# Kernel tuning notes

Hardware: AMD Instinct MI355X
Metric: run time of the kernel (lower is better)

Reference implementation:

```python
import jax, jax.numpy as jnp
import numpy as np


def setup_inputs() -> dict:
    key = jax.random.key(0)
    k1, k2 = jax.random.split(key)
    N, D, K = 131072, 256, 1024
    x = jax.random.normal(k1, (N, D), dtype=jnp.float32)
    centroids = jax.random.normal(k2, (K, D), dtype=jnp.float32)
    return {"x": x, "centroids": centroids}


def reference(x, centroids):
    """Nearest-centroid assignment with euclidean similarity (kmeans_pytorch euc_sim):
        sim[n,k] = 2 * x[n] . c[k] - |x[n]|^2 - |c[k]|^2  ( = -||x[n]-c[k]||^2 )
    Returns (max_sim [N], labels [N]).
    """
    # [N, K] similarity via single GEMM plus broadcast norms
    sim = (2.0 * jnp.einsum('nd,kd->nk', x, centroids)
           - jnp.sum(x * x, axis=-1, keepdims=True)
           - jnp.sum(centroids * centroids, axis=-1)[None, :])
    max_sim = jnp.max(sim, axis=-1)
    labels = jnp.argmax(sim, axis=-1)
    return max_sim, labels
```

## Files before the change

kernel.cpp:

```cpp
#include <hip/hip_runtime.h>

constexpr int N = 131072;
constexpr int D = 256;
constexpr int K = 1024;

constexpr int TM = 128;
constexpr int TK = 128;
constexpr float EPS = 0.08f;

typedef _Float16 f16x8 __attribute__((ext_vector_type(8)));
typedef float f32x4 __attribute__((ext_vector_type(4)));

__device__ _Float16 g_ctile[66 * 8192];

__device__ __forceinline__ float sqf(float a) { return __fmul_rn(a, a); }

__device__ __forceinline__ float np_sumsq128(const float* q) {
    float lane[16];
#pragma unroll
    for (int j = 0; j < 16; j++) {
        const float r0 = __fadd_rn(sqf(q[j]),      sqf(q[64 + j]));
        const float r1 = __fadd_rn(sqf(q[16 + j]), sqf(q[80 + j]));
        const float r2 = __fadd_rn(sqf(q[32 + j]), sqf(q[96 + j]));
        const float r3 = __fadd_rn(sqf(q[48 + j]), sqf(q[112 + j]));
        lane[j] = __fadd_rn(__fadd_rn(r0, r1), __fadd_rn(r2, r3));
    }
    float t[8];
#pragma unroll
    for (int i = 0; i < 8; i++) t[i] = __fadd_rn(lane[i], lane[i + 8]);
    float u[4];
#pragma unroll
    for (int i = 0; i < 4; i++) u[i] = __fadd_rn(t[i], t[i + 4]);
    return __fadd_rn(__fadd_rn(u[0], u[2]), __fadd_rn(u[1], u[3]));
}
__device__ __forceinline__ float np_pw256_sq(const float* p) {
    return __fadd_rn(np_sumsq128(p), np_sumsq128(p + 128));
}

__device__ __forceinline__ float np_dot256(const float* a, const float* b) {
    float A[4] = {0.f, 0.f, 0.f, 0.f};
#pragma unroll 4
    for (int t = 0; t < 16; t++) {
#pragma unroll
        for (int i = 3; i >= 0; i--) {
            const int base = 16 * t + 4 * i;
#pragma unroll
            for (int j = 0; j < 4; j++)
                A[j] = __fadd_rn(A[j], __fmul_rn(a[base + j], b[base + j]));
        }
    }
    return __fadd_rn(__fadd_rn(A[0], A[1]), __fadd_rn(A[2], A[3]));
}

#define SPL(vec, comp, he, le, idx)                                  \
    {                                                                \
        const float fv_ = (vec).comp;                                \
        const _Float16 hh_ = (_Float16)fv_;                          \
        he[idx] = hh_;                                               \
        le[idx] = (_Float16)(fv_ - (float)hh_);                      \
    }

__global__ __launch_bounds__(256) void prep_kernel(const float* __restrict__ c,
                                                   float* __restrict__ cn) {
    const int idx = blockIdx.x * 256 + threadIdx.x;
    const int kglob = idx >> 5;
    const int dslot = idx & 31;
    const int dc = dslot >> 2, kg = dslot & 3;
    const float* src = c + (size_t)kglob * D + dc * 32 + kg * 8;
    const float4 s0 = ((const float4*)src)[0];
    const float4 s1 = ((const float4*)src)[1];
    f16x8 h, l;
    SPL(s0, x, h, l, 0) SPL(s0, y, h, l, 1) SPL(s0, z, h, l, 2) SPL(s0, w, h, l, 3)
    SPL(s1, x, h, l, 4) SPL(s1, y, h, l, 5) SPL(s1, z, h, l, 6) SPL(s1, w, h, l, 7)
    const int kblk = kglob >> 7, krow = kglob & 127;
    const int st = kblk * 8 + dc;
    _Float16* base = g_ctile + (size_t)st * 8192;
    *(f16x8*)&base[kg * 1024 + krow * 8]        = h;
    *(f16x8*)&base[4096 + kg * 1024 + krow * 8] = l;
    if (idx < K) cn[idx] = np_pw256_sq(c + (size_t)idx * D);
}

#define WAITVM(n) asm volatile("s_waitcnt vmcnt(" #n ")" ::: "memory")

__global__ __launch_bounds__(512, 4) void fast_kernel(const float* __restrict__ x,
                                                      const float* __restrict__ c,
                                                      const float* __restrict__ cn,
                                                      float* __restrict__ out,
                                                      int* __restrict__ cnt,
                                                      int* __restrict__ list) {
    __shared__ _Float16 cs[4][8192] __attribute__((aligned(16)));
    __shared__ float cn_sh[K];
    __shared__ float xn_sh[TM];
    __shared__ int   rbi[TM];
    __shared__ int   rok[TM];

    const int t    = threadIdx.x;
    const int n0   = blockIdx.x * TM;
    const int lane = t & 63;
    const int w    = t >> 6;
    const int wrow = w * 16;
    const int lr   = lane & 15;
    const int lg   = lane >> 4;

    const int kbR = blockIdx.x & 7;
    const int dcR = (blockIdx.x >> 3) & 7;
#define PHYS(p_) ((p_) < 64 ? (((((p_) >> 3) + kbR) & 7) << 3) | ((((p_) & 7) + dcR) & 7) : (p_))

#define STAGE(buf_, sidx_)                                                          \
    {                                                                               \
        const _Float16* gp_ = g_ctile + (size_t)(sidx_) * 8192 + t * 8;             \
        _Float16* lp_ = &cs[buf_][t * 8];                                           \
        __builtin_amdgcn_global_load_lds(                                           \
            (const __attribute__((address_space(1))) void*)gp_,                     \
            (__attribute__((address_space(3))) void*)lp_, 16, 0, 0);                \
        __builtin_amdgcn_global_load_lds(                                           \
            (const __attribute__((address_space(1))) void*)(gp_ + 4096),            \
            (__attribute__((address_space(3))) void*)(lp_ + 4096), 16, 0, 0);       \
    }

    STAGE(0, PHYS(0));
    STAGE(1, PHYS(1));

#pragma unroll
    for (int q = 0; q < 2; q++) cn_sh[t + 512 * q] = cn[t + 512 * q];
    if (t < TM) xn_sh[t] = np_pw256_sq(x + (size_t)(n0 + t) * D);

    f16x8 ah[8], al[8];
#pragma unroll
    for (int st = 0; st < 8; st++) {
        const int pst = (st + dcR) & 7;
        const float* src = x + (size_t)(n0 + wrow + lr) * D + pst * 32 + lg * 8;
        const float4 s0 = ((const float4*)src)[0];
        const float4 s1 = ((const float4*)src)[1];
        f16x8 h, l;
        SPL(s0, x, h, l, 0) SPL(s0, y, h, l, 1) SPL(s0, z, h, l, 2) SPL(s0, w, h, l, 3)
        SPL(s1, x, h, l, 4) SPL(s1, y, h, l, 5) SPL(s1, z, h, l, 6) SPL(s1, w, h, l, 7)
        ah[st] = h; al[st] = l;
    }

    float v1[4], v2[4];
    int   i1[4];
#pragma unroll
    for (int s = 0; s < 4; s++) {
        v1[s] = -__builtin_inff(); v2[s] = -__builtin_inff(); i1[s] = 0;
    }

    __syncthreads();

    for (int kb0 = 0; kb0 < 8; kb0++) {
        const int kbE = (kb0 + kbR) & 7;
        f32x4 acc[8];
#pragma unroll
        for (int j = 0; j < 8; j++) acc[j] = (f32x4)(0.f);

#pragma unroll
        for (int dc8 = 0; dc8 < 8; dc8++) {
            const int p2 = kb0 * 8 + dc8 + 2;
            STAGE((dc8 + 2) & 3, PHYS(p2));
            WAITVM(4);
            __builtin_amdgcn_s_barrier();
            __builtin_amdgcn_sched_barrier(0);
            asm volatile("" ::: "memory");

            const _Float16* csb = &cs[dc8 & 3][0];
            __builtin_amdgcn_s_setprio(1);
#pragma unroll
            for (int j = 0; j < 8; j++) {
                const f16x8 bh = *(const f16x8*)&csb[lg * 1024 + (16 * j + lr) * 8];
                const f16x8 bl = *(const f16x8*)&csb[4096 + lg * 1024 + (16 * j + lr) * 8];
                acc[j] = __builtin_amdgcn_mfma_f32_16x16x32_f16(ah[dc8], bh, acc[j], 0, 0, 0);
                acc[j] = __builtin_amdgcn_mfma_f32_16x16x32_f16(al[dc8], bh, acc[j], 0, 0, 0);
                acc[j] = __builtin_amdgcn_mfma_f32_16x16x32_f16(ah[dc8], bl, acc[j], 0, 0, 0);
            }
            __builtin_amdgcn_s_setprio(0);
            asm volatile("" ::: "memory");
        }

#pragma unroll
        for (int j = 0; j < 8; j++) {
            const int kg_ = kbE * TK + 16 * j + lr;
            const float cnj = cn_sh[kg_];
#pragma unroll
            for (int r = 0; r < 4; r++) {
                const float v = 2.0f * acc[j][r] - xn_sh[wrow + 4 * lg + r] - cnj;
                if (v > v1[r])       { v2[r] = v1[r]; v1[r] = v; i1[r] = kg_; }
                else if (v > v2[r])  { v2[r] = v; }
                else if (v == v1[r]) { v2[r] = v; }
            }
        }
    }

#pragma unroll
    for (int r = 0; r < 4; r++) {
        float a1v = v1[r], a2v = v2[r];
        int   ai  = i1[r];
#pragma unroll
        for (int m = 1; m <= 8; m <<= 1) {
            const float ov1 = __shfl_xor(a1v, m);
            const int   oi  = __shfl_xor(ai, m);
            const float ov2 = __shfl_xor(a2v, m);
            if (ov1 > a1v)      { a2v = fmaxf(a1v, ov2); a1v = ov1; ai = oi; }
            else if (ov1 < a1v) { a2v = fmaxf(a2v, ov1); }
            else                { ai = min(ai, oi); a2v = a1v; }
        }
        if (lr == 0) {
            const int row = wrow + 4 * lg + r;
            const int ok = (a1v - a2v >= EPS) ? 1 : 0;
            rbi[row] = ai;
            rok[row] = ok;
            if (!ok) { const int pos = atomicAdd(cnt, 1); list[pos] = n0 + row; }
        }
    }
    __syncthreads();

    if (t < TM && rok[t]) {
        const int row = n0 + t;
        const int bi  = rbi[t];
        const float dot = np_dot256(x + (size_t)row * D, c + (size_t)bi * D);
        const float v = __fsub_rn(__fsub_rn(__fmul_rn(2.0f, dot), xn_sh[t]), cn[bi]);
        out[row]     = v;
        out[N + row] = (float)bi;
    }
}

__global__ __launch_bounds__(256) void fallback_kernel(const float* __restrict__ x,
                                                       const float* __restrict__ c,
                                                       const float* __restrict__ cn,
                                                       float* __restrict__ out,
                                                       const int* __restrict__ cnt,
                                                       const int* __restrict__ list) {
    __shared__ float xrow[D];
    __shared__ float xn_s;
    __shared__ float wv[4];
    __shared__ int   wi[4];
    const int tid = threadIdx.x, lane = tid & 63, w = tid >> 6;
    const int total = *cnt;
    for (int idx = blockIdx.x; idx < total; idx += gridDim.x) {
        const int row = list[idx];
        if (tid < 64) *(float4*)&xrow[4 * tid] = ((const float4*)(x + (size_t)row * D))[tid];
        __syncthreads();
        if (tid == 0) xn_s = np_pw256_sq(xrow);
        __syncthreads();
        const float xn = xn_s;
        float bv = -__builtin_inff();
        int   bi = 0;
#pragma unroll
        for (int j = 0; j < 4; j++) {
            const int k = 4 * tid + j;
            const float dot = np_dot256(xrow, c + (size_t)k * D);
            const float v = __fsub_rn(__fsub_rn(__fmul_rn(2.0f, dot), xn), cn[k]);
            if (v > bv) { bv = v; bi = k; }
        }
#pragma unroll
        for (int m = 1; m <= 32; m <<= 1) {
            const float ov = __shfl_xor(bv, m);
            const int   oi = __shfl_xor(bi, m);
            if (ov > bv || (ov == bv && oi < bi)) { bv = ov; bi = oi; }
        }
        if (lane == 0) { wv[w] = bv; wi[w] = bi; }
        __syncthreads();
        if (tid == 0) {
#pragma unroll
            for (int ww = 1; ww < 4; ww++) {
                if (wv[ww] > bv || (wv[ww] == bv && wi[ww] < bi)) { bv = wv[ww]; bi = wi[ww]; }
            }
            out[row]     = bv;
            out[N + row] = (float)bi;
        }
        __syncthreads();
    }
}

extern "C" void kernel_launch(void* const* d_in, const int* in_sizes, int n_in,
                              void* d_out, int out_size, void* d_ws, size_t ws_size,
                              hipStream_t stream) {
    const float* x = (const float*)d_in[0];
    const float* c = (const float*)d_in[1];
    float* out     = (float*)d_out;
    float* cn = (float*)d_ws;
    int* cnt  = (int*)((char*)d_ws + 4096);
    int* list = (int*)((char*)d_ws + 4608);

    hipMemsetAsync(cnt, 0, sizeof(int), stream);
    prep_kernel<<<128, 256, 0, stream>>>(c, cn);
    fast_kernel<<<N / TM, 512, 0, stream>>>(x, c, cn, out, cnt, list);
    fallback_kernel<<<1024, 256, 0, stream>>>(x, c, cn, out, cnt, list);
}
```

Baseline: 534.7 us.

## Pre-split x into fp16 hi/lo tiles and stream A operand through LDS

Adds a prep pass that converts all of x into pre-tiled fp16 hi/lo blocks in a global scratch buffer. The fast kernel then stages A tiles into LDS with async global_load_lds alongside the centroid tiles, instead of holding 16 register vectors per thread. The LDS ring drops from four buffers to two, with an extra barrier before each refill, and the per-block start rotation is removed. This frees registers and may allow better occupancy, but it costs a full extra read and write of x (about 128MB of fp16 written, then re-read), plus more LDS traffic per step.

Result: slower. 667.7 us (+24.9%).

```diff
diff --git a/kernel.cpp b/kernel.cpp
--- a/kernel.cpp
+++ b/kernel.cpp
@@ -12,6 +12,7 @@
 typedef float f32x4 __attribute__((ext_vector_type(4)));
 
 __device__ _Float16 g_ctile[66 * 8192];
+__device__ _Float16 g_xtile[(size_t)1024 * 8 * 8192];
 
 __device__ __forceinline__ float sqf(float a) { return __fmul_rn(a, a); }
 
@@ -60,24 +61,41 @@
         le[idx] = (_Float16)(fv_ - (float)hh_);                      \
     }
 
-__global__ __launch_bounds__(256) void prep_kernel(const float* __restrict__ c,
+__global__ __launch_bounds__(256) void prep_kernel(const float* __restrict__ x,
+                                                   const float* __restrict__ c,
                                                    float* __restrict__ cn) {
-    const int idx = blockIdx.x * 256 + threadIdx.x;
-    const int kglob = idx >> 5;
-    const int dslot = idx & 31;
-    const int dc = dslot >> 2, kg = dslot & 3;
-    const float* src = c + (size_t)kglob * D + dc * 32 + kg * 8;
-    const float4 s0 = ((const float4*)src)[0];
-    const float4 s1 = ((const float4*)src)[1];
-    f16x8 h, l;
-    SPL(s0, x, h, l, 0) SPL(s0, y, h, l, 1) SPL(s0, z, h, l, 2) SPL(s0, w, h, l, 3)
-    SPL(s1, x, h, l, 4) SPL(s1, y, h, l, 5) SPL(s1, z, h, l, 6) SPL(s1, w, h, l, 7)
-    const int kblk = kglob >> 7, krow = kglob & 127;
-    const int st = kblk * 8 + dc;
-    _Float16* base = g_ctile + (size_t)st * 8192;
-    *(f16x8*)&base[kg * 1024 + krow * 8]        = h;
-    *(f16x8*)&base[4096 + kg * 1024 + krow * 8] = l;
-    if (idx < K) cn[idx] = np_pw256_sq(c + (size_t)idx * D);
+    if (blockIdx.x < 16384) {
+        const int idx = blockIdx.x * 256 + threadIdx.x;
+        const int r = idx >> 5;
+        const int dslot = idx & 31;
+        const int ds = dslot >> 2, kg = dslot & 3;
+        const float* src = x + (size_t)r * D + ds * 32 + kg * 8;
+        const float4 s0 = ((const float4*)src)[0];
+        const float4 s1 = ((const float4*)src)[1];
+        f16x8 h, l;
+        SPL(s0, x, h, l, 0) SPL(s0, y, h, l, 1) SPL(s0, z, h, l, 2) SPL(s0, w, h, l, 3)
+        SPL(s1, x, h, l, 4) SPL(s1, y, h, l, 5) SPL(s1, z, h, l, 6) SPL(s1, w, h, l, 7)
+        const int blk = r >> 7, rrow = r & 127;
+        _Float16* base = g_xtile + (size_t)(blk * 8 + ds) * 8192;
+        *(f16x8*)&base[kg * 1024 + rrow * 8]        = h;
+        *(f16x8*)&base[4096 + kg * 1024 + rrow * 8] = l;
+    } else {
+        const int idx = (blockIdx.x - 16384) * 256 + threadIdx.x;
+        const int kglob = idx >> 5;
+        const int dslot = idx & 31;
+        const int dc = dslot >> 2, kg = dslot & 3;
+        const float* src = c + (size_t)kglob * D + dc * 32 + kg * 8;
+        const float4 s0 = ((const float4*)src)[0];
+        const float4 s1 = ((const float4*)src)[1];
+        f16x8 h, l;
+        SPL(s0, x, h, l, 0) SPL(s0, y, h, l, 1) SPL(s0, z, h, l, 2) SPL(s0, w, h, l, 3)
+        SPL(s1, x, h, l, 4) SPL(s1, y, h, l, 5) SPL(s1, z, h, l, 6) SPL(s1, w, h, l, 7)
+        const int kblk = kglob >> 7, krow = kglob & 127;
+        _Float16* base = g_ctile + (size_t)(kblk * 8 + dc) * 8192;
+        *(f16x8*)&base[kg * 1024 + krow * 8]        = h;
+        *(f16x8*)&base[4096 + kg * 1024 + krow * 8] = l;
+        if (idx < K) cn[idx] = np_pw256_sq(c + (size_t)idx * D);
+    }
 }
 
 #define WAITVM(n) asm volatile("s_waitcnt vmcnt(" #n ")" ::: "memory")
@@ -88,7 +106,8 @@
                                                       float* __restrict__ out,
                                                       int* __restrict__ cnt,
                                                       int* __restrict__ list) {
-    __shared__ _Float16 cs[4][8192] __attribute__((aligned(16)));
+    __shared__ _Float16 as_[2][8192] __attribute__((aligned(16)));
+    __shared__ _Float16 cs[2][8192] __attribute__((aligned(16)));
     __shared__ float cn_sh[K];
     __shared__ float xn_sh[TM];
     __shared__ int   rbi[TM];
@@ -101,12 +120,9 @@
     const int wrow = w * 16;
     const int lr   = lane & 15;
     const int lg   = lane >> 4;
-
-    const int kbR = blockIdx.x & 7;
-    const int dcR = (blockIdx.x >> 3) & 7;
-#define PHYS(p_) ((p_) < 64 ? (((((p_) >> 3) + kbR) & 7) << 3) | ((((p_) & 7) + dcR) & 7) : (p_))
-
-#define STAGE(buf_, sidx_)                                                          \
+    const size_t xbase = (size_t)blockIdx.x * 8 * 8192;
+
+#define STAGE_B(buf_, sidx_)                                                        \
     {                                                                               \
         const _Float16* gp_ = g_ctile + (size_t)(sidx_) * 8192 + t * 8;             \
         _Float16* lp_ = &cs[buf_][t * 8];                                           \
@@ -117,27 +133,25 @@
             (const __attribute__((address_space(1))) void*)(gp_ + 4096),            \
             (__attribute__((address_space(3))) void*)(lp_ + 4096), 16, 0, 0);       \
     }
-
-    STAGE(0, PHYS(0));
-    STAGE(1, PHYS(1));
+#define STAGE_A(buf_, ds_)                                                          \
+    {                                                                               \
+        const _Float16* gp_ = g_xtile + xbase + (size_t)(ds_) * 8192 + t * 8;       \
+        _Float16* lp_ = &as_[buf_][t * 8];                                          \
+        __builtin_amdgcn_global_load_lds(                                           \
+            (const __attribute__((address_space(1))) void*)gp_,                     \
+            (__attribute__((address_space(3))) void*)lp_, 16, 0, 0);                \
+        __builtin_amdgcn_global_load_lds(                                           \
+            (const __attribute__((address_space(1))) void*)(gp_ + 4096),            \
+            (__attribute__((address_space(3))) void*)(lp_ + 4096), 16, 0, 0);       \
+    }
+
+    STAGE_A(0, 0); STAGE_B(0, 0);
+    STAGE_A(1, 1); STAGE_B(1, 1);
 
 #pragma unroll
     for (int q = 0; q < 2; q++) cn_sh[t + 512 * q] = cn[t + 512 * q];
     if (t < TM) xn_sh[t] = np_pw256_sq(x + (size_t)(n0 + t) * D);
 
-    f16x8 ah[8], al[8];
-#pragma unroll
-    for (int st = 0; st < 8; st++) {
-        const int pst = (st + dcR) & 7;
-        const float* src = x + (size_t)(n0 + wrow + lr) * D + pst * 32 + lg * 8;
-        const float4 s0 = ((const float4*)src)[0];
-        const float4 s1 = ((const float4*)src)[1];
-        f16x8 h, l;
-        SPL(s0, x, h, l, 0) SPL(s0, y, h, l, 1) SPL(s0, z, h, l, 2) SPL(s0, w, h, l, 3)
-        SPL(s1, x, h, l, 4) SPL(s1, y, h, l, 5) SPL(s1, z, h, l, 6) SPL(s1, w, h, l, 7)
-        ah[st] = h; al[st] = l;
-    }
-
     float v1[4], v2[4];
     int   i1[4];
 #pragma unroll
@@ -147,38 +161,43 @@
 
     __syncthreads();
 
-    for (int kb0 = 0; kb0 < 8; kb0++) {
-        const int kbE = (kb0 + kbR) & 7;
+    for (int kb = 0; kb < 8; kb++) {
         f32x4 acc[8];
 #pragma unroll
         for (int j = 0; j < 8; j++) acc[j] = (f32x4)(0.f);
 
 #pragma unroll
         for (int dc8 = 0; dc8 < 8; dc8++) {
-            const int p2 = kb0 * 8 + dc8 + 2;
-            STAGE((dc8 + 2) & 3, PHYS(p2));
+            const int p = kb * 8 + dc8;
             WAITVM(4);
             __builtin_amdgcn_s_barrier();
             __builtin_amdgcn_sched_barrier(0);
             asm volatile("" ::: "memory");
 
-            const _Float16* csb = &cs[dc8 & 3][0];
+            const _Float16* asb = &as_[dc8 & 1][0];
+            const _Float16* csb = &cs[dc8 & 1][0];
+            const f16x8 ah = *(const f16x8*)&asb[lg * 1024 + (wrow + lr) * 8];
+            const f16x8 al = *(const f16x8*)&asb[4096 + lg * 1024 + (wrow + lr) * 8];
             __builtin_amdgcn_s_setprio(1);
 #pragma unroll
             for (int j = 0; j < 8; j++) {
                 const f16x8 bh = *(const f16x8*)&csb[lg * 1024 + (16 * j + lr) * 8];
                 const f16x8 bl = *(const f16x8*)&csb[4096 + lg * 1024 + (16 * j + lr) * 8];
-                acc[j] = __builtin_amdgcn_mfma_f32_16x16x32_f16(ah[dc8], bh, acc[j], 0, 0, 0);
-                acc[j] = __builtin_amdgcn_mfma_f32_16x16x32_f16(al[dc8], bh, acc[j], 0, 0, 0);
-                acc[j] = __builtin_amdgcn_mfma_f32_16x16x32_f16(ah[dc8], bl, acc[j], 0, 0, 0);
+                acc[j] = __builtin_amdgcn_mfma_f32_16x16x32_f16(ah, bh, acc[j], 0, 0, 0);
+                acc[j] = __builtin_amdgcn_mfma_f32_16x16x32_f16(al, bh, acc[j], 0, 0, 0);
+                acc[j] = __builtin_amdgcn_mfma_f32_16x16x32_f16(ah, bl, acc[j], 0, 0, 0);
             }
             __builtin_amdgcn_s_setprio(0);
             asm volatile("" ::: "memory");
+            __builtin_amdgcn_s_barrier();
+            asm volatile("" ::: "memory");
+            STAGE_A(dc8 & 1, (dc8 + 2) & 7);
+            STAGE_B(dc8 & 1, p + 2);
         }
 
 #pragma unroll
         for (int j = 0; j < 8; j++) {
-            const int kg_ = kbE * TK + 16 * j + lr;
+            const int kg_ = kb * TK + 16 * j + lr;
             const float cnj = cn_sh[kg_];
 #pragma unroll
             for (int r = 0; r < 4; r++) {
@@ -282,7 +301,7 @@
     int* list = (int*)((char*)d_ws + 4608);
 
     hipMemsetAsync(cnt, 0, sizeof(int), stream);
-    prep_kernel<<<128, 256, 0, stream>>>(c, cn);
+    prep_kernel<<<16512, 256, 0, stream>>>(x, c, cn);
     fast_kernel<<<N / TM, 512, 0, stream>>>(x, c, cn, out, cnt, list);
     fallback_kernel<<<1024, 256, 0, stream>>>(x, c, cn, out, cnt, list);
 }
```
